# Performance work log

Hardware: AMD Instinct MI355X
Metric: run time of the kernel (lower is better)

## Reference

```python
import jax, jax.numpy as jnp
import numpy as np

HEADS = 8
DIM_HEAD = 64
DIM = 512
CTX_DIM = 512
INNER = HEADS * DIM_HEAD  # 512
EPS = 1e-5


def layernorm(x, g):
    # repo-style LayerNorm: learnable gain g only, no bias, biased variance
    mean = jnp.mean(x, axis=-1, keepdims=True)
    var = jnp.var(x, axis=-1, keepdims=True)
    return (x - mean) * jax.lax.rsqrt(var + EPS) * g


def setup_inputs() -> dict:
    key = jax.random.key(0)
    ks = jax.random.split(key, 8)
    b, n, m = 2, 4096, 4096
    x = jax.random.normal(ks[0], (b, n, DIM), dtype=jnp.float32)
    context = jax.random.normal(ks[1], (b, m, CTX_DIM), dtype=jnp.float32)
    mask = jax.random.bernoulli(ks[2], 0.9, (b, m))  # bool [b, m]
    # parameters
    g_x = jnp.ones((DIM,), dtype=jnp.float32)
    null_kv = jax.random.normal(ks[3], (2, DIM_HEAD), dtype=jnp.float32)
    Wq = jax.random.normal(ks[4], (DIM, INNER), dtype=jnp.float32) * (DIM ** -0.5)
    Wkv = jax.random.normal(ks[5], (CTX_DIM, 2 * INNER), dtype=jnp.float32) * (CTX_DIM ** -0.5)
    Wo = jax.random.normal(ks[6], (INNER, DIM), dtype=jnp.float32) * (INNER ** -0.5)
    g_out = jnp.ones((DIM,), dtype=jnp.float32)
    return {"x": x, "context": context, "mask": mask, "g_x": g_x,
            "null_kv": null_kv, "Wq": Wq, "Wkv": Wkv, "Wo": Wo, "g_out": g_out}


def reference(x, context, mask, g_x, null_kv, Wq, Wkv, Wo, g_out):
    b, n, _ = x.shape
    m = context.shape[1]
    scale = DIM_HEAD ** (-0.5)  # cosine_sim=False

    xn = layernorm(x, g_x)
    ctx = context  # norm_context=False -> Identity

    q = (xn @ Wq).reshape(b, n, HEADS, DIM_HEAD)          # b n h d
    kv = (ctx @ Wkv).reshape(b, m, 2, HEADS, DIM_HEAD)     # b m 2 h d
    k, v = kv[:, :, 0], kv[:, :, 1]                        # b m h d

    # prepend the null kv token (shared across b, h)
    nk = jnp.broadcast_to(null_kv[0], (b, 1, HEADS, DIM_HEAD))
    nv = jnp.broadcast_to(null_kv[1], (b, 1, HEADS, DIM_HEAD))
    k = jnp.concatenate([nk, k], axis=1)                   # b (m+1) h d
    v = jnp.concatenate([nv, v], axis=1)

    s = jnp.sqrt(jnp.float32(scale))
    q = q * s
    k = k * s

    sim = jnp.einsum('bihd,bjhd->bhij', q, k)              # b h n (m+1)
    max_neg = -jnp.finfo(sim.dtype).max
    full_mask = jnp.pad(mask, ((0, 0), (1, 0)), constant_values=True)  # null token visible
    sim = jnp.where(full_mask[:, None, None, :], sim, max_neg)

    attn = jax.nn.softmax(sim.astype(jnp.float32), axis=-1).astype(sim.dtype)
    out = jnp.einsum('bhij,bjhd->bihd', attn, v).reshape(b, n, INNER)
    out = out @ Wo
    return layernorm(out, g_out)
```

## Files before the change

### kernel.cpp

```cpp
#include <hip/hip_runtime.h>
#include <cfloat>

typedef unsigned short u16;
typedef unsigned int u32;
typedef __bf16 v8bf16 __attribute__((ext_vector_type(8)));
typedef float v4f32 __attribute__((ext_vector_type(4)));
typedef float v16f32 __attribute__((ext_vector_type(16)));

#define MPAD 4224
#define QKS 0.42466090f
#define GRPS 1024

__device__ __forceinline__ u16 f2bf(float f) {
  union { float f; u32 u; } v; v.f = f;
  u32 u = v.u;
  u32 r = (u + 0x7FFFu + ((u >> 16) & 1u)) >> 16;
  return (u16)r;
}

__device__ __forceinline__ u32 pkbf(float lo, float hi) {
  union { float f; u32 u; } a, c;
  a.f = lo; c.f = hi;
  return __builtin_amdgcn_perm(c.u, a.u, 0x07060302);
}

__device__ __forceinline__ float asf(u32 u) {
  union { u32 u; float f; } v; v.u = u; return v.f;
}

__device__ __forceinline__ void exppack2(v16f32& sA, v16f32& sB, float& lst,
                                         v8bf16 pf[4]) {
  float rsum = 0.f;
#pragma unroll
  for (int i = 0; i < 16; i++) { float p = __builtin_amdgcn_exp2f(sA[i]); sA[i] = p; rsum += p; }
#pragma unroll
  for (int i = 0; i < 16; i++) { float p = __builtin_amdgcn_exp2f(sB[i]); sB[i] = p; rsum += p; }
  float a2 = rsum, b2 = rsum;
  asm("v_permlane32_swap_b32 %0, %1" : "+v"(a2), "+v"(b2));
  lst += a2 + b2;
#pragma unroll
  for (int kc = 0; kc < 2; kc++) {
    v16f32& s = kc ? sB : sA;
#pragma unroll
    for (int s16 = 0; s16 < 2; s16++) {
      u32 w0 = pkbf(s[s16 * 8 + 0], s[s16 * 8 + 1]);
      u32 w1 = pkbf(s[s16 * 8 + 2], s[s16 * 8 + 3]);
      u32 w2 = pkbf(s[s16 * 8 + 4], s[s16 * 8 + 5]);
      u32 w3 = pkbf(s[s16 * 8 + 6], s[s16 * 8 + 7]);
      asm("v_permlane32_swap_b32 %0, %1" : "+v"(w0), "+v"(w2));
      asm("v_permlane32_swap_b32 %0, %1" : "+v"(w1), "+v"(w3));
      union { u32 u[4]; v8bf16 v; } pu;
      pu.u[0] = w0; pu.u[1] = w1; pu.u[2] = w2; pu.u[3] = w3;
      pf[kc * 2 + s16] = pu.v;
    }
  }
}

__global__ __launch_bounds__(256) void prep_all(
    const void* __restrict__ mask, float* __restrict__ mp,
    const float* __restrict__ Wq, const float* __restrict__ Wkv,
    const float* __restrict__ Wo, u16* __restrict__ WqT,
    u16* __restrict__ WkvT, u16* __restrict__ WoT,
    const float* __restrict__ x, const float* __restrict__ g,
    u16* __restrict__ xn, const float4* __restrict__ ctx, u16* __restrict__ cb,
    const float* __restrict__ nullkv, u16* __restrict__ KVt) {
  int bb = blockIdx.x;
  int tid = threadIdx.x;
  if (bb < 33) {
    __shared__ int sflag;
    if (tid == 0) sflag = 0;
    __syncthreads();
    const unsigned char* mb = (const unsigned char*)mask;
    int loc = 0;
#pragma unroll
    for (int k = 0; k < 32; k++) {
      int i = tid * 32 + k;
      if ((i & 3) && mb[i]) loc = 1;
    }
    if (loc) sflag = 1;
    __syncthreads();
    int isbyte = sflag;
    int i = bb * 256 + tid;
    if (i >= 2 * MPAD) return;
    int b = i / MPAD, p = i - b * MPAD;
    float v;
    if (p == 0) v = 0.f;
    else if (p <= 4096) {
      int j = b * 4096 + (p - 1);
      int on = isbyte ? (((const unsigned char*)mask)[j] != 0)
                      : (((const int*)mask)[j] != 0);
      v = on ? 0.f : -1e38f;
    } else v = -1e38f;
    mp[i] = v;
  } else if (bb < 1057) {
    __shared__ float tile[32][33];
    int t = bb - 33;
    const float* in; u16* out; int N; float scale; int base;
    if (t < 256)      { in = Wq;  out = WqT;  N = 512;  scale = QKS; base = t; }
    else if (t < 768) { in = Wkv; out = WkvT; N = 1024; scale = 1.f; base = t - 256; }
    else              { in = Wo;  out = WoT;  N = 512;  scale = 1.f; base = t - 768; }
    const int K = 512;
    int ntiles = N >> 5;
    int bx = base % ntiles, by = base / ntiles;
    int n0 = bx * 32, k0 = by * 32;
    int c = tid & 31, r8 = tid >> 5;
#pragma unroll
    for (int i = 0; i < 4; i++) {
      int r = r8 + i * 8;
      tile[r][c] = in[(size_t)(k0 + r) * N + n0 + c];
    }
    __syncthreads();
#pragma unroll
    for (int i = 0; i < 4; i++) {
      int r = r8 + i * 8;
      out[(size_t)(n0 + r) * K + k0 + c] = f2bf(tile[c][r] * scale);
    }
  } else if (bb < 7201) {
    int local = bb - 1057;
    if (local < 2048) {
      int lane = tid & 63, w = tid >> 6;
      int row = local * 4 + w;
      const float* p = x + (size_t)row * 512 + lane * 8;
      float4 f0 = *(const float4*)p;
      float4 f1 = *(const float4*)(p + 4);
      float v[8] = {f0.x, f0.y, f0.z, f0.w, f1.x, f1.y, f1.z, f1.w};
      float sum = 0.f, sq = 0.f;
#pragma unroll
      for (int i = 0; i < 8; i++) { sum += v[i]; sq += v[i] * v[i]; }
#pragma unroll
      for (int m = 1; m < 64; m <<= 1) { sum += __shfl_xor(sum, m); sq += __shfl_xor(sq, m); }
      float mean = sum * (1.f / 512.f);
      float var = sq * (1.f / 512.f) - mean * mean;
      float rstd = rsqrtf(var + 1e-5f);
      const float* gp = g + lane * 8;
      u16 o[8];
#pragma unroll
      for (int i = 0; i < 8; i++) o[i] = f2bf((v[i] - mean) * rstd * gp[i]);
      *(uint4*)&xn[(size_t)row * 512 + lane * 8] = *(uint4*)o;
    } else {
      int i = (local - 2048) * 256 + tid;
      float4 f = ctx[i];
      u16 o[4] = {f2bf(f.x), f2bf(f.y), f2bf(f.z), f2bf(f.w)};
      *(uint2*)&cb[(size_t)i * 4] = *(uint2*)o;
    }
  } else {
    int bh = bb - 7201;
    size_t tb64 = ((size_t)bh * 66 + 64) * 8192;
    uint4 z = make_uint4(0, 0, 0, 0);
    for (int i = tid; i < 2048; i += 256)
      *(uint4*)&KVt[tb64 + (size_t)i * 8] = z;
    size_t tb0 = (size_t)bh * 66 * 8192;
    if (tid < 64) {
      int d = tid;
      KVt[tb0 + (size_t)(d >> 3) * 512 + (d & 7)] = f2bf(nullkv[d] * QKS);
      KVt[tb0 + 4096 + (size_t)d * 8] = f2bf(nullkv[64 + d]);
    }
  }
}

__global__ __launch_bounds__(256) void ln_to_f32(const float* __restrict__ in,
    const float* __restrict__ g, float* __restrict__ out) {
  int lane = threadIdx.x & 63, w = threadIdx.x >> 6;
  int row = blockIdx.x * 4 + w;
  const float* p = in + (size_t)row * 512 + lane * 8;
  float4 f0 = *(const float4*)p;
  float4 f1 = *(const float4*)(p + 4);
  float v[8] = {f0.x, f0.y, f0.z, f0.w, f1.x, f1.y, f1.z, f1.w};
  float sum = 0.f, sq = 0.f;
#pragma unroll
  for (int i = 0; i < 8; i++) { sum += v[i]; sq += v[i] * v[i]; }
#pragma unroll
  for (int m = 1; m < 64; m <<= 1) { sum += __shfl_xor(sum, m); sq += __shfl_xor(sq, m); }
  float mean = sum * (1.f / 512.f);
  float var = sq * (1.f / 512.f) - mean * mean;
  float rstd = rsqrtf(var + 1e-5f);
  const float* gp = g + lane * 8;
  float o[8];
#pragma unroll
  for (int i = 0; i < 8; i++) o[i] = (v[i] - mean) * rstd * gp[i];
  float* q = out + (size_t)row * 512 + lane * 8;
  *(float4*)q = make_float4(o[0], o[1], o[2], o[3]);
  *(float4*)(q + 4) = make_float4(o[4], o[5], o[6], o[7]);
}

__device__ __forceinline__ void gemm_core(const u16* __restrict__ A,
    const u16* __restrict__ Bt, u16* __restrict__ outb,
    u16* __restrict__ KVt, int Ncols, int mode, int bidx,
    u16* As , u16* Bs ) {
  int tiles_n = Ncols >> 7;
  int n0 = (bidx % tiles_n) * 128;
  int m0 = (bidx / tiles_n) * 128;
  int tid = threadIdx.x;
  int lane = tid & 63, w = tid >> 6, quad = lane >> 4, l15 = lane & 15;
  int wr = w >> 1, wc = w & 1;
  int srow = tid >> 2, scol = (tid & 3) * 8;
  v4f32 acc[4][4];
#pragma unroll
  for (int i = 0; i < 4; i++)
#pragma unroll
    for (int j = 0; j < 4; j++) acc[i][j] = (v4f32){0.f, 0.f, 0.f, 0.f};

  for (int k0 = 0; k0 < 512; k0 += 32) {
    __syncthreads();
    __builtin_amdgcn_global_load_lds((const u32*)&A[(size_t)(m0 + srow) * 512 + k0 + scol],
                                     (u32*)&As[tid * 8], 16, 0, 0);
    __builtin_amdgcn_global_load_lds((const u32*)&A[(size_t)(m0 + 64 + srow) * 512 + k0 + scol],
                                     (u32*)&As[64 * 32 + tid * 8], 16, 0, 0);
    __builtin_amdgcn_global_load_lds((const u32*)&Bt[(size_t)(n0 + srow) * 512 + k0 + scol],
                                     (u32*)&Bs[tid * 8], 16, 0, 0);
    __builtin_amdgcn_global_load_lds((const u32*)&Bt[(size_t)(n0 + 64 + srow) * 512 + k0 + scol],
                                     (u32*)&Bs[64 * 32 + tid * 8], 16, 0, 0);
    __syncthreads();
    v8bf16 af[4], bf[4];
#pragma unroll
    for (int i = 0; i < 4; i++)
      af[i] = *(const v8bf16*)&As[(wr * 64 + i * 16 + l15) * 32 + quad * 8];
#pragma unroll
    for (int j = 0; j < 4; j++)
      bf[j] = *(const v8bf16*)&Bs[(wc * 64 + j * 16 + l15) * 32 + quad * 8];
#pragma unroll
    for (int i = 0; i < 4; i++)
#pragma unroll
      for (int j = 0; j < 4; j++)
        acc[i][j] = __builtin_amdgcn_mfma_f32_16x16x32_bf16(af[i], bf[j], acc[i][j], 0, 0, 0);
  }
#pragma unroll
  for (int i = 0; i < 4; i++) {
    int rbase = m0 + wr * 64 + i * 16 + quad * 4;
#pragma unroll
    for (int j = 0; j < 4; j++) {
      int col = n0 + wc * 64 + j * 16 + l15;
#pragma unroll
      for (int r = 0; r < 4; r++) {
        float v = acc[i][j][r];
        int row = rbase + r;
        if (mode == 0) {
          outb[(size_t)row * 512 + col] = f2bf(v);
        } else {
          int b2 = row >> 12, mr = row & 4095;
          int kk = mr + 1, kt = kk >> 6, kl = kk & 63;
          int kvsel = col >> 9, hh = (col >> 6) & 7, d = col & 63;
          size_t tb = ((size_t)(b2 * 8 + hh) * 66 + kt) * 8192;
          if (kvsel == 0) {
            int chunk = (((d >> 4) * 2 + ((d >> 3) & 1)) * 2 + (kl >> 5)) * 32 + (kl & 31);
            KVt[tb + (size_t)chunk * 8 + (d & 7)] = f2bf(v * QKS);
          } else {
            int chunk = (((kl >> 4) * 2 + ((kl >> 3) & 1)) * 2 + (d >> 5)) * 32 + (d & 31);
            KVt[tb + 4096 + (size_t)chunk * 8 + (kl & 7)] = f2bf(v);
          }
        }
      }
    }
  }
}

__global__ __launch_bounds__(256) void gemm_qkv(const u16* __restrict__ xn,
    const u16* __restrict__ WqT, u16* __restrict__ qb,
    const u16* __restrict__ cb, const u16* __restrict__ WkvT,
    u16* __restrict__ KVt) {
  __shared__ __attribute__((aligned(16))) u16 As[128 * 32];
  __shared__ __attribute__((aligned(16))) u16 Bs[128 * 32];
  int bb = blockIdx.x;
  if (bb < 256) gemm_core(xn, WqT, qb, nullptr, 512, 0, bb, As, Bs);
  else          gemm_core(cb, WkvT, nullptr, KVt, 1024, 1, bb - 256, As, Bs);
}

__global__ __launch_bounds__(256) void gemm_o(const u16* __restrict__ A,
    const u16* __restrict__ Bt, float* __restrict__ outf) {
  __shared__ __attribute__((aligned(16))) u16 As[128 * 32];
  __shared__ __attribute__((aligned(16))) u16 Bs[64 * 32];
  int n0 = (blockIdx.x & 7) * 64;
  int m0 = (blockIdx.x >> 3) * 128;
  int tid = threadIdx.x;
  int lane = tid & 63, w = tid >> 6, quad = lane >> 4, l15 = lane & 15;
  int srow = tid >> 2, scol = (tid & 3) * 8;
  v4f32 acc[2][4];
#pragma unroll
  for (int i = 0; i < 2; i++)
#pragma unroll
    for (int j = 0; j < 4; j++) acc[i][j] = (v4f32){0.f, 0.f, 0.f, 0.f};

  for (int k0 = 0; k0 < 512; k0 += 32) {
    __syncthreads();
    __builtin_amdgcn_global_load_lds((const u32*)&A[(size_t)(m0 + srow) * 512 + k0 + scol],
                                     (u32*)&As[tid * 8], 16, 0, 0);
    __builtin_amdgcn_global_load_lds((const u32*)&A[(size_t)(m0 + 64 + srow) * 512 + k0 + scol],
                                     (u32*)&As[64 * 32 + tid * 8], 16, 0, 0);
    __builtin_amdgcn_global_load_lds((const u32*)&Bt[(size_t)(n0 + srow) * 512 + k0 + scol],
                                     (u32*)&Bs[tid * 8], 16, 0, 0);
    __syncthreads();
    v8bf16 af[2], bf[4];
#pragma unroll
    for (int i = 0; i < 2; i++)
      af[i] = *(const v8bf16*)&As[(w * 32 + i * 16 + l15) * 32 + quad * 8];
#pragma unroll
    for (int j = 0; j < 4; j++)
      bf[j] = *(const v8bf16*)&Bs[(j * 16 + l15) * 32 + quad * 8];
#pragma unroll
    for (int i = 0; i < 2; i++)
#pragma unroll
      for (int j = 0; j < 4; j++)
        acc[i][j] = __builtin_amdgcn_mfma_f32_16x16x32_bf16(af[i], bf[j], acc[i][j], 0, 0, 0);
  }
#pragma unroll
  for (int i = 0; i < 2; i++) {
    int rbase = m0 + w * 32 + i * 16 + quad * 4;
#pragma unroll
    for (int j = 0; j < 4; j++) {
      int col = n0 + j * 16 + l15;
#pragma unroll
      for (int r = 0; r < 4; r++)
        outf[(size_t)(rbase + r) * 512 + col] = acc[i][j][r];
    }
  }
}

__global__ __launch_bounds__(256, 2) void attn_kernel(const u16* __restrict__ q,
    const u16* __restrict__ KVt, const float* __restrict__ maskbias,
    u32* __restrict__ Opart, float* __restrict__ lbuf) {
  int obid = blockIdx.x;
  int bid = (obid & 7) * 64 + (obid >> 3);
  int qt = bid & 15, bhs = bid >> 4;
  int s_p = bhs & 1, bh = bhs >> 1;
  int b = bh >> 3, hh = bh & 7;
  int tid = threadIdx.x, lane = tid & 63, w = tid >> 6;
  int m31 = lane & 31, h = (lane >> 5) & 1;
  int grp = (bh * 16 + qt) * 4 + w;
  int q0 = qt * 256 + w * 64;

  v8bf16 qf[2][4];
#pragma unroll
  for (int qg = 0; qg < 2; qg++) {
    const u16* qp = q + (size_t)(b * 4096 + q0 + qg * 32 + m31) * 512 + hh * 64 + h * 8;
#pragma unroll
    for (int ks = 0; ks < 4; ks++) qf[qg][ks] = *(const v8bf16*)&qp[ks * 16];
  }

  v16f32 acc[2][2];
#pragma unroll
  for (int qg = 0; qg < 2; qg++)
#pragma unroll
    for (int db = 0; db < 2; db++)
#pragma unroll
      for (int i = 0; i < 16; i++) acc[qg][db][i] = 0.f;
  float l_st[2] = {0.f, 0.f};

  const u16* kvb = KVt + (size_t)bh * 66 * 8192 + (size_t)(h * 64 + m31) * 8;
  const float* mg = maskbias + b * MPAD;
  int kt0 = s_p * 33;

  for (int kt = kt0; kt < kt0 + 33; ++kt) {
    const u16* tb = kvb + (size_t)kt * 8192;
    v8bf16 kf[4][2];
#pragma unroll
    for (int ks = 0; ks < 4; ks++)
#pragma unroll
      for (int kc = 0; kc < 2; kc++)
        kf[ks][kc] = *(const v8bf16*)&tb[ks * 1024 + kc * 256];
    v16f32 bias_s[2];
#pragma unroll
    for (int kc = 0; kc < 2; kc++)
#pragma unroll
      for (int gg = 0; gg < 4; gg++) {
        float4 bv = *(const float4*)&mg[kt * 64 + kc * 32 + gg * 8 + h * 4];
        bias_s[kc][gg * 4 + 0] = bv.x;
        bias_s[kc][gg * 4 + 1] = bv.y;
        bias_s[kc][gg * 4 + 2] = bv.z;
        bias_s[kc][gg * 4 + 3] = bv.w;
      }

    v8bf16 pf[2][4];
    {
      v16f32 s0 = bias_s[0], s1 = bias_s[1];
      __builtin_amdgcn_s_setprio(1);
#pragma unroll
      for (int ks = 0; ks < 4; ks++) {
        s0 = __builtin_amdgcn_mfma_f32_32x32x16_bf16(kf[ks][0], qf[0][ks], s0, 0, 0, 0);
        s1 = __builtin_amdgcn_mfma_f32_32x32x16_bf16(kf[ks][1], qf[0][ks], s1, 0, 0, 0);
      }
      __builtin_amdgcn_s_setprio(0);
      exppack2(s0, s1, l_st[0], pf[0]);
    }
    __builtin_amdgcn_s_setprio(1);
#pragma unroll
    for (int ks = 0; ks < 4; ks++) {
      bias_s[0] = __builtin_amdgcn_mfma_f32_32x32x16_bf16(kf[ks][0], qf[1][ks], bias_s[0], 0, 0, 0);
      bias_s[1] = __builtin_amdgcn_mfma_f32_32x32x16_bf16(kf[ks][1], qf[1][ks], bias_s[1], 0, 0, 0);
    }
    __builtin_amdgcn_s_setprio(0);
    exppack2(bias_s[0], bias_s[1], l_st[1], pf[1]);

    v8bf16 vf[4][2];
#pragma unroll
    for (int jb = 0; jb < 4; jb++)
#pragma unroll
      for (int db = 0; db < 2; db++)
        vf[jb][db] = *(const v8bf16*)&tb[4096 + jb * 1024 + db * 256];

    __builtin_amdgcn_s_setprio(1);
#pragma unroll
    for (int qg = 0; qg < 2; qg++)
#pragma unroll
      for (int jb = 0; jb < 4; jb++)
#pragma unroll
        for (int db = 0; db < 2; db++)
          acc[qg][db] = __builtin_amdgcn_mfma_f32_32x32x16_bf16(vf[jb][db], pf[qg][jb], acc[qg][db], 0, 0, 0);
    __builtin_amdgcn_s_setprio(0);
  }

  size_t ob = (size_t)(s_p * GRPS + grp) * 2048;
#pragma unroll
  for (int qg = 0; qg < 2; qg++)
#pragma unroll
    for (int db = 0; db < 2; db++)
#pragma unroll
      for (int rp = 0; rp < 8; rp++)
        Opart[ob + qg * 1024 + (size_t)(db * 8 + rp) * 64 + lane] =
            pkbf(acc[qg][db][2 * rp], acc[qg][db][2 * rp + 1]);
  if (h == 0) {
    lbuf[(size_t)(s_p * GRPS + grp) * 64 + m31] = l_st[0];
    lbuf[(size_t)(s_p * GRPS + grp) * 64 + 32 + m31] = l_st[1];
  }
}

__global__ __launch_bounds__(256) void attn_combine(const u32* __restrict__ Opart,
    const float* __restrict__ lbuf, u16* __restrict__ attnO) {
  __shared__ __attribute__((aligned(16))) u16 tl[4][2176];
  int tid = threadIdx.x, lane = tid & 63, w4 = tid >> 6;
  int m31 = lane & 31, h = (lane >> 5) & 1;
  int gq = blockIdx.x * 4 + w4;
  int qg = gq & 1, grp = gq >> 1;
  int w = grp & 3, qt = (grp >> 2) & 15, bh = grp >> 6;
  int b = bh >> 3, hh = bh & 7;

  float l0 = lbuf[(size_t)grp * 64 + qg * 32 + m31];
  float l1 = lbuf[(size_t)(GRPS + grp) * 64 + qg * 32 + m31];
  float inv = 1.f / (l0 + l1);

#pragma unroll
  for (int db = 0; db < 2; db++)
#pragma unroll
    for (int rp = 0; rp < 8; rp++) {
      u32 a = Opart[(size_t)grp * 2048 + qg * 1024 + (db * 8 + rp) * 64 + lane];
      u32 c = Opart[(size_t)(GRPS + grp) * 2048 + qg * 1024 + (db * 8 + rp) * 64 + lane];
      float fe = (asf(a << 16) + asf(c << 16)) * inv;
      float fo = (asf(a & 0xFFFF0000u) + asf(c & 0xFFFF0000u)) * inv;
      int reg = 2 * rp;
      int d0 = (reg & 3) + 8 * (reg >> 2) + 4 * h + 32 * db;
      *(u32*)&tl[w4][m31 * 68 + d0] = pkbf(fe, fo);
    }
  __builtin_amdgcn_s_waitcnt(0);
  int q0 = qt * 256 + w * 64 + qg * 32;
#pragma unroll
  for (int t2 = 0; t2 < 4; t2++) {
    int row = t2 * 8 + (lane >> 3), ch = lane & 7;
    uint4 val = *(uint4*)&tl[w4][row * 68 + ch * 8];
    *(uint4*)&attnO[(size_t)(b * 4096 + q0 + row) * 512 + hh * 64 + ch * 8] = val;
  }
}

extern "C" void kernel_launch(void* const* d_in, const int* in_sizes, int n_in,
                              void* d_out, int out_size, void* d_ws, size_t ws_size,
                              hipStream_t stream) {
  const float* x       = (const float*)d_in[0];
  const float* context = (const float*)d_in[1];
  const void*  mask    = d_in[2];
  const float* g_x     = (const float*)d_in[3];
  const float* null_kv = (const float*)d_in[4];
  const float* Wq      = (const float*)d_in[5];
  const float* Wkv     = (const float*)d_in[6];
  const float* Wo      = (const float*)d_in[7];
  const float* g_out   = (const float*)d_in[8];

  char* w = (char*)d_ws;
  size_t off = 0;
  auto alloc = [&](size_t bytes) { size_t o = off; off = (off + bytes + 255) & ~(size_t)255; return o; };

  u16* WqT    = (u16*)(w + alloc((size_t)512 * 512 * 2));
  u16* WkvT   = (u16*)(w + alloc((size_t)1024 * 512 * 2));
  u16* WoT    = (u16*)(w + alloc((size_t)512 * 512 * 2));
  float* mp   = (float*)(w + alloc((size_t)2 * MPAD * 4));
  u16* KVt    = (u16*)(w + alloc((size_t)16 * 66 * 8192 * 2));
  u16* qb     = (u16*)(w + alloc((size_t)8192 * 512 * 2));
  u16* aO     = (u16*)(w + alloc((size_t)8192 * 512 * 2));
  size_t xn_off = alloc((size_t)8192 * 512 * 2);
  size_t cb_off = alloc((size_t)8192 * 512 * 2);
  float* lbb  = (float*)(w + alloc((size_t)2 * GRPS * 64 * 4));
  u16* xn   = (u16*)(w + xn_off);
  u16* cb   = (u16*)(w + cb_off);
  u32* Opart = (u32*)(w + xn_off);
  float* OP  = (float*)(w + xn_off);

  prep_all<<<7217, 256, 0, stream>>>(mask, mp, Wq, Wkv, Wo, WqT, WkvT, WoT,
                                     x, g_x, xn, (const float4*)context, cb,
                                     null_kv, KVt);

  gemm_qkv<<<768, 256, 0, stream>>>(xn, WqT, qb, cb, WkvT, KVt);

  attn_kernel<<<512, 256, 0, stream>>>(qb, KVt, mp, Opart, lbb);
  attn_combine<<<512, 256, 0, stream>>>(Opart, lbb, aO);

  gemm_o<<<512, 256, 0, stream>>>(aO, WoT, OP);
  ln_to_f32<<<2048, 256, 0, stream>>>(OP, g_out, (float*)d_out);
}
```

Before: 232.8 us.

## Fuse attention combine, output projection and final layernorm into one kernel

Replaces the separate split-softmax combine, output-projection GEMM and layernorm kernels with a single kernel. Each block merges the two partial attention outputs for 64 rows across all heads into shared memory, multiplies them by the full 512-column Wo held in 32 accumulators per wave, and applies the layernorm in registers before writing the fp32 output. This removes two launches and the round trips of the bf16 attention output and the fp32 pre-norm buffer through global memory. In exchange only 128 blocks are launched, each using about 100 KB of LDS and many accumulator registers, with no double buffering of the Wo tiles. That may leave much of the GPU idle and make the GEMM latency-bound.

```diff
diff --git a/kernel.cpp b/kernel.cpp
--- a/kernel.cpp
+++ b/kernel.cpp
@@ -158,31 +158,6 @@
   }
 }
 
-__global__ __launch_bounds__(256) void ln_to_f32(const float* __restrict__ in,
-    const float* __restrict__ g, float* __restrict__ out) {
-  int lane = threadIdx.x & 63, w = threadIdx.x >> 6;
-  int row = blockIdx.x * 4 + w;
-  const float* p = in + (size_t)row * 512 + lane * 8;
-  float4 f0 = *(const float4*)p;
-  float4 f1 = *(const float4*)(p + 4);
-  float v[8] = {f0.x, f0.y, f0.z, f0.w, f1.x, f1.y, f1.z, f1.w};
-  float sum = 0.f, sq = 0.f;
-#pragma unroll
-  for (int i = 0; i < 8; i++) { sum += v[i]; sq += v[i] * v[i]; }
-#pragma unroll
-  for (int m = 1; m < 64; m <<= 1) { sum += __shfl_xor(sum, m); sq += __shfl_xor(sq, m); }
-  float mean = sum * (1.f / 512.f);
-  float var = sq * (1.f / 512.f) - mean * mean;
-  float rstd = rsqrtf(var + 1e-5f);
-  const float* gp = g + lane * 8;
-  float o[8];
-#pragma unroll
-  for (int i = 0; i < 8; i++) o[i] = (v[i] - mean) * rstd * gp[i];
-  float* q = out + (size_t)row * 512 + lane * 8;
-  *(float4*)q = make_float4(o[0], o[1], o[2], o[3]);
-  *(float4*)(q + 4) = make_float4(o[4], o[5], o[6], o[7]);
-}
-
 __device__ __forceinline__ void gemm_core(const u16* __restrict__ A,
     const u16* __restrict__ Bt, u16* __restrict__ outb,
     u16* __restrict__ KVt, int Ncols, int mode, int bidx,
@@ -265,56 +240,6 @@
   else          gemm_core(cb, WkvT, nullptr, KVt, 1024, 1, bb - 256, As, Bs);
 }
 
-__global__ __launch_bounds__(256) void gemm_o(const u16* __restrict__ A,
-    const u16* __restrict__ Bt, float* __restrict__ outf) {
-  __shared__ __attribute__((aligned(16))) u16 As[128 * 32];
-  __shared__ __attribute__((aligned(16))) u16 Bs[64 * 32];
-  int n0 = (blockIdx.x & 7) * 64;
-  int m0 = (blockIdx.x >> 3) * 128;
-  int tid = threadIdx.x;
-  int lane = tid & 63, w = tid >> 6, quad = lane >> 4, l15 = lane & 15;
-  int srow = tid >> 2, scol = (tid & 3) * 8;
-  v4f32 acc[2][4];
-#pragma unroll
-  for (int i = 0; i < 2; i++)
-#pragma unroll
-    for (int j = 0; j < 4; j++) acc[i][j] = (v4f32){0.f, 0.f, 0.f, 0.f};
-
-  for (int k0 = 0; k0 < 512; k0 += 32) {
-    __syncthreads();
-    __builtin_amdgcn_global_load_lds((const u32*)&A[(size_t)(m0 + srow) * 512 + k0 + scol],
-                                     (u32*)&As[tid * 8], 16, 0, 0);
-    __builtin_amdgcn_global_load_lds((const u32*)&A[(size_t)(m0 + 64 + srow) * 512 + k0 + scol],
-                                     (u32*)&As[64 * 32 + tid * 8], 16, 0, 0);
-    __builtin_amdgcn_global_load_lds((const u32*)&Bt[(size_t)(n0 + srow) * 512 + k0 + scol],
-                                     (u32*)&Bs[tid * 8], 16, 0, 0);
-    __syncthreads();
-    v8bf16 af[2], bf[4];
-#pragma unroll
-    for (int i = 0; i < 2; i++)
-      af[i] = *(const v8bf16*)&As[(w * 32 + i * 16 + l15) * 32 + quad * 8];
-#pragma unroll
-    for (int j = 0; j < 4; j++)
-      bf[j] = *(const v8bf16*)&Bs[(j * 16 + l15) * 32 + quad * 8];
-#pragma unroll
-    for (int i = 0; i < 2; i++)
-#pragma unroll
-      for (int j = 0; j < 4; j++)
-        acc[i][j] = __builtin_amdgcn_mfma_f32_16x16x32_bf16(af[i], bf[j], acc[i][j], 0, 0, 0);
-  }
-#pragma unroll
-  for (int i = 0; i < 2; i++) {
-    int rbase = m0 + w * 32 + i * 16 + quad * 4;
-#pragma unroll
-    for (int j = 0; j < 4; j++) {
-      int col = n0 + j * 16 + l15;
-#pragma unroll
-      for (int r = 0; r < 4; r++)
-        outf[(size_t)(rbase + r) * 512 + col] = acc[i][j][r];
-    }
-  }
-}
-
 __global__ __launch_bounds__(256, 2) void attn_kernel(const u16* __restrict__ q,
     const u16* __restrict__ KVt, const float* __restrict__ maskbias,
     u32* __restrict__ Opart, float* __restrict__ lbuf) {
@@ -423,39 +348,85 @@
   }
 }
 
-__global__ __launch_bounds__(256) void attn_combine(const u32* __restrict__ Opart,
-    const float* __restrict__ lbuf, u16* __restrict__ attnO) {
-  __shared__ __attribute__((aligned(16))) u16 tl[4][2176];
-  int tid = threadIdx.x, lane = tid & 63, w4 = tid >> 6;
+__global__ __launch_bounds__(256) void tail3(const u32* __restrict__ Opart,
+    const float* __restrict__ lbuf, const u16* __restrict__ WoT,
+    const float* __restrict__ g, float* __restrict__ out) {
+  __shared__ __attribute__((aligned(16))) u16 As[64 * 520];
+  __shared__ __attribute__((aligned(16))) u16 Bs[512 * 32];
+  int bid = blockIdx.x;
+  int tid = threadIdx.x;
+  int w4 = tid >> 6, lane = tid & 63;
   int m31 = lane & 31, h = (lane >> 5) & 1;
-  int gq = blockIdx.x * 4 + w4;
-  int qg = gq & 1, grp = gq >> 1;
-  int w = grp & 3, qt = (grp >> 2) & 15, bh = grp >> 6;
-  int b = bh >> 3, hh = bh & 7;
-
-  float l0 = lbuf[(size_t)grp * 64 + qg * 32 + m31];
-  float l1 = lbuf[(size_t)(GRPS + grp) * 64 + qg * 32 + m31];
-  float inv = 1.f / (l0 + l1);
-
-#pragma unroll
-  for (int db = 0; db < 2; db++)
-#pragma unroll
-    for (int rp = 0; rp < 8; rp++) {
-      u32 a = Opart[(size_t)grp * 2048 + qg * 1024 + (db * 8 + rp) * 64 + lane];
-      u32 c = Opart[(size_t)(GRPS + grp) * 2048 + qg * 1024 + (db * 8 + rp) * 64 + lane];
-      float fe = (asf(a << 16) + asf(c << 16)) * inv;
-      float fo = (asf(a & 0xFFFF0000u) + asf(c & 0xFFFF0000u)) * inv;
-      int reg = 2 * rp;
-      int d0 = (reg & 3) + 8 * (reg >> 2) + 4 * h + 32 * db;
-      *(u32*)&tl[w4][m31 * 68 + d0] = pkbf(fe, fo);
-    }
-  __builtin_amdgcn_s_waitcnt(0);
-  int q0 = qt * 256 + w * 64 + qg * 32;
-#pragma unroll
-  for (int t2 = 0; t2 < 4; t2++) {
-    int row = t2 * 8 + (lane >> 3), ch = lane & 7;
-    uint4 val = *(uint4*)&tl[w4][row * 68 + ch * 8];
-    *(uint4*)&attnO[(size_t)(b * 4096 + q0 + row) * 512 + hh * 64 + ch * 8] = val;
+  int b = bid >> 6, qt = (bid >> 2) & 15, w = bid & 3;
+  size_t rowbase = (size_t)b * 4096 + qt * 256 + w * 64;
+
+#pragma unroll
+  for (int i = 0; i < 4; i++) {
+    int u = i * 4 + w4;
+    int hh = u >> 1, qg = u & 1;
+    int grp = (b * 8 + hh) * 64 + qt * 4 + w;
+    float l0 = lbuf[(size_t)grp * 64 + qg * 32 + m31];
+    float l1 = lbuf[(size_t)(GRPS + grp) * 64 + qg * 32 + m31];
+    float inv = 1.f / (l0 + l1);
+#pragma unroll
+    for (int db = 0; db < 2; db++)
+#pragma unroll
+      for (int rp = 0; rp < 8; rp++) {
+        u32 a = Opart[(size_t)grp * 2048 + qg * 1024 + (db * 8 + rp) * 64 + lane];
+        u32 c = Opart[(size_t)(GRPS + grp) * 2048 + qg * 1024 + (db * 8 + rp) * 64 + lane];
+        float fe = (asf(a << 16) + asf(c << 16)) * inv;
+        float fo = (asf(a & 0xFFFF0000u) + asf(c & 0xFFFF0000u)) * inv;
+        int reg = 2 * rp;
+        int d0 = (reg & 3) + 8 * (reg >> 2) + 4 * h + 32 * db;
+        *(u32*)&As[(qg * 32 + m31) * 520 + hh * 64 + d0] = pkbf(fe, fo);
+      }
+  }
+
+  int quad = lane >> 4, l15 = lane & 15;
+  int srow = tid >> 2, scol = (tid & 3) * 8;
+  v4f32 acc[32];
+#pragma unroll
+  for (int j = 0; j < 32; j++) acc[j] = (v4f32){0.f, 0.f, 0.f, 0.f};
+
+  for (int k0 = 0; k0 < 512; k0 += 32) {
+    __syncthreads();
+#pragma unroll
+    for (int v = 0; v < 8; v++)
+      __builtin_amdgcn_global_load_lds((const u32*)&WoT[(size_t)(v * 64 + srow) * 512 + k0 + scol],
+                                       (u32*)&Bs[(size_t)v * 2048 + tid * 8], 16, 0, 0);
+    __syncthreads();
+    v8bf16 af = *(const v8bf16*)&As[(w4 * 16 + l15) * 520 + k0 + quad * 8];
+#pragma unroll
+    for (int j = 0; j < 32; j++) {
+      v8bf16 bf = *(const v8bf16*)&Bs[(j * 16 + l15) * 32 + quad * 8];
+      acc[j] = __builtin_amdgcn_mfma_f32_16x16x32_bf16(af, bf, acc[j], 0, 0, 0);
+    }
+  }
+
+  float rs[4] = {0.f, 0.f, 0.f, 0.f}, sq[4] = {0.f, 0.f, 0.f, 0.f};
+#pragma unroll
+  for (int j = 0; j < 32; j++)
+#pragma unroll
+    for (int r = 0; r < 4; r++) { float v = acc[j][r]; rs[r] += v; sq[r] += v * v; }
+#pragma unroll
+  for (int m = 1; m < 16; m <<= 1)
+#pragma unroll
+    for (int r = 0; r < 4; r++) { rs[r] += __shfl_xor(rs[r], m); sq[r] += __shfl_xor(sq[r], m); }
+  float mean[4], rstd[4];
+#pragma unroll
+  for (int r = 0; r < 4; r++) {
+    mean[r] = rs[r] * (1.f / 512.f);
+    float var = sq[r] * (1.f / 512.f) - mean[r] * mean[r];
+    rstd[r] = rsqrtf(var + 1e-5f);
+  }
+#pragma unroll
+  for (int j = 0; j < 32; j++) {
+    float gv = g[j * 16 + l15];
+#pragma unroll
+    for (int r = 0; r < 4; r++) {
+      size_t row = rowbase + w4 * 16 + quad * 4 + r;
+      out[row * 512 + j * 16 + l15] = (acc[j][r] - mean[r]) * rstd[r] * gv;
+    }
   }
 }
 
@@ -489,7 +460,7 @@
   u16* xn   = (u16*)(w + xn_off);
   u16* cb   = (u16*)(w + cb_off);
   u32* Opart = (u32*)(w + xn_off);
-  float* OP  = (float*)(w + xn_off);
+  (void)aO;
 
   prep_all<<<7217, 256, 0, stream>>>(mask, mp, Wq, Wkv, Wo, WqT, WkvT, WoT,
                                      x, g_x, xn, (const float4*)context, cb,
@@ -498,8 +469,6 @@
   gemm_qkv<<<768, 256, 0, stream>>>(xn, WqT, qb, cb, WkvT, KVt);
 
   attn_kernel<<<512, 256, 0, stream>>>(qb, KVt, mp, Opart, lbb);
-  attn_combine<<<512, 256, 0, stream>>>(Opart, lbb, aO);
-
-  gemm_o<<<512, 256, 0, stream>>>(aO, WoT, OP);
-  ln_to_f32<<<2048, 256, 0, stream>>>(OP, g_out, (float*)d_out);
-}
+
+  tail3<<<128, 256, 0, stream>>>(Opart, lbb, WoT, g_out, (float*)d_out);
+}
```

Result: no change. 234.8 us (+0.8%).
